# Kernel optimization log

Hardware: AMD Instinct MI355X
Metric: run time of the kernel (lower is better)

## Reference

```python
import jax, jax.numpy as jnp
import numpy as np

D_MODEL = 1024
NHEAD = 16
D_HEAD = D_MODEL // NHEAD


def setup_inputs() -> dict:
    key = jax.random.key(0)
    ks = jax.random.split(key, 11)
    B, S = 4, 1024
    s = 1.0 / np.sqrt(D_MODEL)
    inp = {
        'q_in': jax.random.normal(ks[0], (B, S, D_MODEL), jnp.float32),
        'k_in': jax.random.normal(ks[1], (B, S, D_MODEL), jnp.float32),
        'v_in': jax.random.normal(ks[2], (B, S, D_MODEL), jnp.float32),
        'Wq': jax.random.normal(ks[3], (D_MODEL, D_MODEL), jnp.float32) * s,
        'bq': jnp.zeros((D_MODEL,), jnp.float32),
        'Wk': jax.random.normal(ks[4], (D_MODEL, D_MODEL), jnp.float32) * s,
        'bk': jnp.zeros((D_MODEL,), jnp.float32),
        'Wv': jax.random.normal(ks[5], (D_MODEL, D_MODEL), jnp.float32) * s,
        'bv': jnp.zeros((D_MODEL,), jnp.float32),
        'Wo': jax.random.normal(ks[6], (D_MODEL, D_MODEL), jnp.float32) * s,
        'bo': jnp.zeros((D_MODEL,), jnp.float32),
    }
    return inp


def reference(q_in, k_in, v_in, Wq, bq, Wk, bk, Wv, bv, Wo, bo):
    B, Sq, _ = q_in.shape
    Sk = k_in.shape[1]
    # Linear projections (torch Linear: x @ W.T + b; here W stored as [in, out])
    Q = q_in @ Wq + bq
    K = k_in @ Wk + bk
    V = v_in @ Wv + bv
    # [B, H, S, Dh]
    Qh = Q.reshape(B, Sq, NHEAD, D_HEAD).transpose(0, 2, 1, 3)
    Kh = K.reshape(B, Sk, NHEAD, D_HEAD).transpose(0, 2, 1, 3)
    Vh = V.reshape(B, Sk, NHEAD, D_HEAD).transpose(0, 2, 1, 3)
    scores = jnp.einsum('bhqd,bhkd->bhqk', Qh, Kh) / jnp.sqrt(jnp.float32(D_HEAD))
    attn_weights = jax.nn.softmax(scores, axis=-1)
    attn = jnp.einsum('bhqk,bhkd->bhqd', attn_weights, Vh)
    attn = attn.transpose(0, 2, 1, 3).reshape(B, Sq, D_MODEL)
    out = attn @ Wo + bo
    return out
```

## Files before the change

kernel.cpp:

```cpp
#include <hip/hip_runtime.h>
#include <hip/hip_bf16.h>
#include <cstdint>
#include <cstddef>

typedef __bf16 bf16_t;
typedef __bf16 bf16x8 __attribute__((ext_vector_type(8)));
typedef __bf16 bf16x4 __attribute__((ext_vector_type(4)));
typedef float f32x4 __attribute__((ext_vector_type(4)));

#define DM 1024
#define NHEAD 16
#define DHEAD 64

#define QSCALE 0.18033688011112042f
#define PSHIFT 4.0f
#define RS 72

__device__ __forceinline__ void gload_lds16(const void* g, void* l) {
    __builtin_amdgcn_global_load_lds(
        (const __attribute__((address_space(1))) void*)g,
        (__attribute__((address_space(3))) void*)l,
        16, 0, 0);
}

__device__ __forceinline__ uint4 cvt8(float4 lo, float4 hi) {
    union { bf16_t b[8]; uint4 u; } o;
    o.b[0] = (bf16_t)lo.x; o.b[1] = (bf16_t)lo.y; o.b[2] = (bf16_t)lo.z; o.b[3] = (bf16_t)lo.w;
    o.b[4] = (bf16_t)hi.x; o.b[5] = (bf16_t)hi.y; o.b[6] = (bf16_t)hi.z; o.b[7] = (bf16_t)hi.w;
    return o.u;
}

__global__ void prep(
    const float* __restrict__ q_in, const float* __restrict__ k_in, const float* __restrict__ v_in,
    bf16_t* __restrict__ Xq, bf16_t* __restrict__ Xk, bf16_t* __restrict__ Xv,
    const float* __restrict__ w0, const float* __restrict__ w1,
    const float* __restrict__ w2, const float* __restrict__ w3,
    bf16_t* __restrict__ t0, bf16_t* __restrict__ t1,
    bf16_t* __restrict__ t2, bf16_t* __restrict__ t3)
{
    __shared__ float tile[32][33];
    int id = blockIdx.x;
    if (id < 6144) {
        int plane = id >> 11;
        int blk = id & 2047;
        const float* x = plane == 0 ? q_in : plane == 1 ? k_in : v_in;
        bf16_t* y      = plane == 0 ? Xq   : plane == 1 ? Xk   : Xv;
        int i = (blk * 256 + threadIdx.x) * 8;
        float4 lo = *(const float4*)&x[i];
        float4 hi = *(const float4*)&x[i + 4];
        *(uint4*)&y[i] = cvt8(lo, hi);
    } else {
        int t = id - 6144;
        int zi = t >> 10;
        int blk = t & 1023;
        const float* w = zi == 0 ? w0 : zi == 1 ? w1 : zi == 2 ? w2 : w3;
        bf16_t* wt     = zi == 0 ? t0 : zi == 1 ? t1 : zi == 2 ? t2 : t3;
        int bx = (blk & 31) * 32;
        int by = (blk >> 5) * 32;
        int tx = threadIdx.x & 31, ty = threadIdx.x >> 5;
        for (int j = 0; j < 32; j += 8)
            tile[ty + j][tx] = w[(size_t)(by + ty + j) * DM + bx + tx];
        __syncthreads();
        for (int j = 0; j < 32; j += 8)
            wt[(size_t)(bx + ty + j) * DM + by + tx] = (bf16_t)tile[tx][ty + j];
    }
}

template <int MODE>
__device__ __forceinline__ void gemm_body(
    const bf16_t* __restrict__ A, const bf16_t* __restrict__ Bt,
    const float* __restrict__ bias, float scale,
    float* __restrict__ Cf, bf16_t* __restrict__ Cb,
    int r0, int c0, bf16_t* AsP, bf16_t* BsP)
{
    const int K = 1024;
    int tid  = threadIdx.x;
    int wave = tid >> 6;
    int lane = tid & 63;
    int quad = lane >> 4;
    int ln   = lane & 15;
    int wr   = wave >> 1;
    int wc   = wave & 1;

    f32x4 acc[4][4];
    for (int rb = 0; rb < 4; rb++)
        for (int cb = 0; cb < 4; cb++)
            acc[rb][cb] = (f32x4){0.f, 0.f, 0.f, 0.f};

    int sr = tid >> 2;
    int sk = (tid & 3) * 8;

    const bf16_t* gA0 = &A[(size_t)(r0 + sr) * K + sk];
    const bf16_t* gA1 = gA0 + (size_t)64 * K;
    const bf16_t* gB0 = &Bt[(size_t)(c0 + sr) * K + sk];
    const bf16_t* gB1 = gB0 + (size_t)64 * K;
    char* lA = (char*)AsP + wave * 1024;
    char* lB = (char*)BsP + wave * 1024;

    gload_lds16(gA0, lA);
    gload_lds16(gA1, lA + 4096);
    gload_lds16(gB0, lB);
    gload_lds16(gB1, lB + 4096);
    __syncthreads();

    int cur = 0;
    for (int k0 = 0; k0 < K; k0 += 32) {
        int nxt = cur ^ 1;
        if (k0 + 32 < K) {
            int off = nxt * 8192;
            gload_lds16(gA0 + k0 + 32, lA + off);
            gload_lds16(gA1 + k0 + 32, lA + off + 4096);
            gload_lds16(gB0 + k0 + 32, lB + off);
            gload_lds16(gB1 + k0 + 32, lB + off + 4096);
        }
        const bf16_t* Ab = AsP + cur * 4096;
        const bf16_t* Bb = BsP + cur * 4096;

        bf16x8 af[4], bfv[4];
        for (int rb = 0; rb < 4; rb++)
            af[rb] = *(const bf16x8*)&Ab[(wr * 64 + rb * 16 + ln) * 32 + quad * 8];
        for (int cb = 0; cb < 4; cb++)
            bfv[cb] = *(const bf16x8*)&Bb[(wc * 64 + cb * 16 + ln) * 32 + quad * 8];
        for (int rb = 0; rb < 4; rb++)
            for (int cb = 0; cb < 4; cb++)
                acc[rb][cb] = __builtin_amdgcn_mfma_f32_16x16x32_bf16(af[rb], bfv[cb], acc[rb][cb], 0, 0, 0);

        __syncthreads();
        cur = nxt;
    }

    for (int rb = 0; rb < 4; rb++) {
        for (int cb = 0; cb < 4; cb++) {
            int C = c0 + wc * 64 + cb * 16 + ln;
            for (int r = 0; r < 4; r++) {
                int R = r0 + wr * 64 + rb * 16 + quad * 4 + r;
                float v = acc[rb][cb][r];
                if (MODE == 0) {
                    Cf[(size_t)R * DM + C] = v + bias[C];
                } else if (MODE == 1) {
                    int b = R >> 10, s = R & 1023;
                    int h = C >> 6,  d = C & 63;
                    Cb[(((size_t)b * NHEAD + h) * 1024 + s) * DHEAD + d] =
                        (bf16_t)((v + bias[C]) * scale);
                } else {
                    Cb[((size_t)(C >> 10) * 1024 + R) * 1024 + (C & 1023)] =
                        (bf16_t)(v + bias[R]);
                }
            }
        }
    }
}

__global__ __launch_bounds__(256) void gemm_qkv(
    const bf16_t* __restrict__ Xq, const bf16_t* __restrict__ Xk, const bf16_t* __restrict__ Xv,
    const bf16_t* __restrict__ Wtq, const bf16_t* __restrict__ Wtk, const bf16_t* __restrict__ Wtv,
    const float* __restrict__ bq, const float* __restrict__ bk, const float* __restrict__ bv,
    bf16_t* __restrict__ Qd, bf16_t* __restrict__ Kd, bf16_t* __restrict__ Vt)
{
    __shared__ __align__(16) bf16_t As[2 * 128 * 32];
    __shared__ __align__(16) bf16_t Bs[2 * 128 * 32];
    int z = blockIdx.z;
    if (z == 0) {
        gemm_body<1>(Xq, Wtq, bq, QSCALE, nullptr, Qd,
                     blockIdx.x * 128, blockIdx.y * 128, As, Bs);
    } else if (z == 1) {
        gemm_body<1>(Xk, Wtk, bk, 1.0f, nullptr, Kd,
                     blockIdx.x * 128, blockIdx.y * 128, As, Bs);
    } else {
        gemm_body<2>(Wtv, Xv, bv, 1.0f, nullptr, Vt,
                     blockIdx.y * 128, blockIdx.x * 128, As, Bs);
    }
}

__global__ __launch_bounds__(256) void gemm_out(
    const bf16_t* __restrict__ At, const bf16_t* __restrict__ Wto,
    const float* __restrict__ bo, float* __restrict__ out)
{
    const int K = 1024;
    __shared__ __align__(16) bf16_t As[2 * 64 * 32];
    __shared__ __align__(16) bf16_t Bs[2 * 128 * 32];

    int tid  = threadIdx.x;
    int wave = tid >> 6;
    int lane = tid & 63;
    int quad = lane >> 4;
    int ln   = lane & 15;

    int r0 = blockIdx.x * 64;
    int c0 = blockIdx.y * 128;

    f32x4 acc[4][2];
    for (int rb = 0; rb < 4; rb++)
        for (int cb = 0; cb < 2; cb++)
            acc[rb][cb] = (f32x4){0.f, 0.f, 0.f, 0.f};

    int sr = tid >> 2;
    int sk = (tid & 3) * 8;

    const bf16_t* gA0 = At  + (size_t)(r0 + sr) * K + sk;
    const bf16_t* gB0 = Wto + (size_t)(c0 + sr) * K + sk;
    const bf16_t* gB1 = gB0 + (size_t)64 * K;
    char* lA = (char*)As + wave * 1024;
    char* lB = (char*)Bs + wave * 1024;

    gload_lds16(gA0, lA);
    gload_lds16(gB0, lB);
    gload_lds16(gB1, lB + 4096);
    __syncthreads();

    int cur = 0;
    for (int k0 = 0; k0 < K; k0 += 32) {
        int nxt = cur ^ 1;
        if (k0 + 32 < K) {
            gload_lds16(gA0 + k0 + 32, lA + nxt * 4096);
            gload_lds16(gB0 + k0 + 32, lB + nxt * 8192);
            gload_lds16(gB1 + k0 + 32, lB + nxt * 8192 + 4096);
        }
        const bf16_t* Ab = As + cur * 2048;
        const bf16_t* Bb = Bs + cur * 4096;

        bf16x8 af[4], bfv[2];
        for (int rb = 0; rb < 4; rb++)
            af[rb] = *(const bf16x8*)&Ab[(rb * 16 + ln) * 32 + quad * 8];
        for (int cb = 0; cb < 2; cb++)
            bfv[cb] = *(const bf16x8*)&Bb[(wave * 32 + cb * 16 + ln) * 32 + quad * 8];
        for (int rb = 0; rb < 4; rb++)
            for (int cb = 0; cb < 2; cb++)
                acc[rb][cb] = __builtin_amdgcn_mfma_f32_16x16x32_bf16(af[rb], bfv[cb], acc[rb][cb], 0, 0, 0);

        __syncthreads();
        cur = nxt;
    }

    for (int rb = 0; rb < 4; rb++) {
        for (int cb = 0; cb < 2; cb++) {
            int C = c0 + wave * 32 + cb * 16 + ln;
            float bn = bo[C];
            for (int r = 0; r < 4; r++) {
                int R = r0 + rb * 16 + quad * 4 + r;
                out[(size_t)R * DM + C] = acc[rb][cb][r] + bn;
            }
        }
    }
}

__global__ __launch_bounds__(256) void attn5(
    const bf16_t* __restrict__ Q,
    const bf16_t* __restrict__ K,
    const bf16_t* __restrict__ Vt,
    bf16_t* __restrict__ O)
{
    __shared__ __align__(16) bf16_t Ks[64 * RS];
    __shared__ __align__(16) bf16_t Vs[64 * RS];
    __shared__ __align__(16) bf16_t Ps[4][16 * RS];

    int tid  = threadIdx.x;
    int wave = tid >> 6;
    int lane = tid & 63;
    int quad = lane >> 4;
    int ln   = lane & 15;

    int bh = blockIdx.x;
    int q0w = blockIdx.y * 64 + wave * 16;

    const bf16_t* Qb = Q  + (size_t)bh * 65536;
    const bf16_t* Kb = K  + (size_t)bh * 65536;
    const bf16_t* Vb = Vt + (size_t)bh * 65536;

    int srow = tid >> 3;
    int scol = (tid & 7) * 8;
    const bf16_t* gK0 = Kb + (size_t)srow * 64 + scol;
    const bf16_t* gK1 = gK0 + 32 * 64;
    const bf16_t* gV0 = Vb + (size_t)srow * 1024 + scol;
    const bf16_t* gV1 = gV0 + 32 * 1024;

    bf16x8 aq0 = *(const bf16x8*)&Qb[(size_t)(q0w + ln) * 64 + quad * 8];
    bf16x8 aq1 = *(const bf16x8*)&Qb[(size_t)(q0w + ln) * 64 + 32 + quad * 8];

    uint4 rK0 = *(const uint4*)gK0;
    uint4 rK1 = *(const uint4*)gK1;
    uint4 rV0 = *(const uint4*)gV0;
    uint4 rV1 = *(const uint4*)gV1;

    float l_lane = 0.f;
    f32x4 o_acc[4];
    for (int cb = 0; cb < 4; cb++) o_acc[cb] = (f32x4){0.f, 0.f, 0.f, 0.f};

    bf16_t* Pw = Ps[wave];

    for (int kt = 0; kt < 16; kt++) {
        __syncthreads();
        *(uint4*)&Ks[srow * RS + scol]        = rK0;
        *(uint4*)&Ks[(32 + srow) * RS + scol] = rK1;
        *(uint4*)&Vs[srow * RS + scol]        = rV0;
        *(uint4*)&Vs[(32 + srow) * RS + scol] = rV1;
        __syncthreads();

        if (kt < 15) {
            gK0 += 4096; gK1 += 4096; gV0 += 64; gV1 += 64;
            rK0 = *(const uint4*)gK0;
            rK1 = *(const uint4*)gK1;
            rV0 = *(const uint4*)gV0;
            rV1 = *(const uint4*)gV1;
        }

        f32x4 sc[4];
        for (int kb = 0; kb < 4; kb++) {
            bf16x8 kf0 = *(const bf16x8*)&Ks[(kb * 16 + ln) * RS + quad * 8];
            bf16x8 kf1 = *(const bf16x8*)&Ks[(kb * 16 + ln) * RS + 32 + quad * 8];
            f32x4 a = (f32x4){0.f, 0.f, 0.f, 0.f};
            a = __builtin_amdgcn_mfma_f32_16x16x32_bf16(kf0, aq0, a, 0, 0, 0);
            a = __builtin_amdgcn_mfma_f32_16x16x32_bf16(kf1, aq1, a, 0, 0, 0);
            sc[kb] = a;
        }

        for (int kb = 0; kb < 4; kb++) {
            float p0 = __builtin_amdgcn_exp2f(sc[kb][0] - PSHIFT);
            float p1 = __builtin_amdgcn_exp2f(sc[kb][1] - PSHIFT);
            float p2 = __builtin_amdgcn_exp2f(sc[kb][2] - PSHIFT);
            float p3 = __builtin_amdgcn_exp2f(sc[kb][3] - PSHIFT);
            l_lane += (p0 + p1) + (p2 + p3);
            bf16x4 pk = (bf16x4){(bf16_t)p0, (bf16_t)p1, (bf16_t)p2, (bf16_t)p3};
            *(bf16x4*)&Pw[ln * RS + kb * 16 + quad * 4] = pk;
        }

        for (int kc = 0; kc < 2; kc++) {
            bf16x8 ap = *(const bf16x8*)&Pw[ln * RS + kc * 32 + quad * 8];
            for (int cb = 0; cb < 4; cb++) {
                bf16x8 vf = *(const bf16x8*)&Vs[(cb * 16 + ln) * RS + kc * 32 + quad * 8];
                o_acc[cb] = __builtin_amdgcn_mfma_f32_16x16x32_bf16(ap, vf, o_acc[cb], 0, 0, 0);
            }
        }
    }

    float l = l_lane;
    l += __shfl_xor(l, 16);
    l += __shfl_xor(l, 32);
    float invq[4];
    for (int r = 0; r < 4; r++)
        invq[r] = 1.f / __shfl(l, quad * 4 + r);

    int b = bh >> 4, h = bh & 15;
    for (int cb = 0; cb < 4; cb++) {
        for (int r = 0; r < 4; r++) {
            int q = q0w + quad * 4 + r;
            int d = cb * 16 + ln;
            O[((size_t)b * 1024 + q) * DM + h * 64 + d] = (bf16_t)(o_acc[cb][r] * invq[r]);
        }
    }
}

extern "C" void kernel_launch(void* const* d_in, const int* in_sizes, int n_in,
                              void* d_out, int out_size, void* d_ws, size_t ws_size,
                              hipStream_t stream) {
    const float* q_in = (const float*)d_in[0];
    const float* k_in = (const float*)d_in[1];
    const float* v_in = (const float*)d_in[2];
    const float* Wq   = (const float*)d_in[3];
    const float* bq   = (const float*)d_in[4];
    const float* Wk   = (const float*)d_in[5];
    const float* bk   = (const float*)d_in[6];
    const float* Wv   = (const float*)d_in[7];
    const float* bv   = (const float*)d_in[8];
    const float* Wo   = (const float*)d_in[9];
    const float* bo   = (const float*)d_in[10];

    char* ws = (char*)d_ws;
    const size_t MB = 1024ull * 1024ull;
    bf16_t* Xq  = (bf16_t*)(ws);
    bf16_t* Xk  = (bf16_t*)(ws + 8 * MB);
    bf16_t* Xv  = (bf16_t*)(ws + 16 * MB);
    bf16_t* Wtq = (bf16_t*)(ws + 24 * MB);
    bf16_t* Wtk = (bf16_t*)(ws + 26 * MB);
    bf16_t* Wtv = (bf16_t*)(ws + 28 * MB);
    bf16_t* Wto = (bf16_t*)(ws + 30 * MB);
    bf16_t* Qd  = (bf16_t*)(ws + 32 * MB);
    bf16_t* Kd  = (bf16_t*)(ws + 40 * MB);
    bf16_t* Vt  = (bf16_t*)(ws + 48 * MB);
    bf16_t* At  = Xq;

    prep<<<10240, 256, 0, stream>>>(q_in, k_in, v_in, Xq, Xk, Xv,
                                    Wq, Wk, Wv, Wo, Wtq, Wtk, Wtv, Wto);

    gemm_qkv<<<dim3(32, 8, 3), 256, 0, stream>>>(Xq, Xk, Xv,
                                                 Wtq, Wtk, Wtv, bq, bk, bv, Qd, Kd, Vt);

    attn5<<<dim3(64, 16), 256, 0, stream>>>(Qd, Kd, Vt, At);

    gemm_out<<<dim3(64, 8), 256, 0, stream>>>(At, Wto, bo, (float*)d_out);
}
```

Before: 208.4 us.

## Double query rows per attention wave and widen weight-transpose tiles

The attention kernel now has each wave process 32 query rows instead of 16, so every K/V tile staged in shared memory is reused by twice as many queries. This halves the grid and the K/V global traffic per query. Separately, the weight transpose in the prep kernel uses 64x64 tiles with 16-byte vectorized bf16 stores instead of 32x32 tiles with scalar stores. The cost is more registers per wave and fewer attention blocks in flight, which may lower occupancy and latency hiding.

```diff
diff --git a/kernel.cpp b/kernel.cpp
--- a/kernel.cpp
+++ b/kernel.cpp
@@ -38,7 +38,7 @@
     bf16_t* __restrict__ t0, bf16_t* __restrict__ t1,
     bf16_t* __restrict__ t2, bf16_t* __restrict__ t3)
 {
-    __shared__ float tile[32][33];
+    __shared__ float tile[64][65];
     int id = blockIdx.x;
     if (id < 6144) {
         int plane = id >> 11;
@@ -51,18 +51,25 @@
         *(uint4*)&y[i] = cvt8(lo, hi);
     } else {
         int t = id - 6144;
-        int zi = t >> 10;
-        int blk = t & 1023;
+        int zi = t >> 8;
+        int blk = t & 255;
         const float* w = zi == 0 ? w0 : zi == 1 ? w1 : zi == 2 ? w2 : w3;
         bf16_t* wt     = zi == 0 ? t0 : zi == 1 ? t1 : zi == 2 ? t2 : t3;
-        int bx = (blk & 31) * 32;
-        int by = (blk >> 5) * 32;
-        int tx = threadIdx.x & 31, ty = threadIdx.x >> 5;
-        for (int j = 0; j < 32; j += 8)
+        int bx = (blk & 15) * 64;
+        int by = (blk >> 4) * 64;
+        int tx = threadIdx.x & 63, ty = threadIdx.x >> 6;
+        for (int j = 0; j < 64; j += 4)
             tile[ty + j][tx] = w[(size_t)(by + ty + j) * DM + bx + tx];
         __syncthreads();
-        for (int j = 0; j < 32; j += 8)
-            wt[(size_t)(bx + ty + j) * DM + by + tx] = (bf16_t)tile[tx][ty + j];
+        int nl = threadIdx.x >> 3;
+        int kl = (threadIdx.x & 7) * 8;
+        for (int j = 0; j < 64; j += 32) {
+            int n = nl + j;
+            union { bf16_t b[8]; uint4 u; } o;
+            for (int i = 0; i < 8; i++)
+                o.b[i] = (bf16_t)tile[kl + i][n];
+            *(uint4*)&wt[(size_t)(bx + n) * DM + by + kl] = o.u;
+        }
     }
 }
 
@@ -244,7 +251,7 @@
     }
 }
 
-__global__ __launch_bounds__(256) void attn5(
+__global__ __launch_bounds__(256) void attn6(
     const bf16_t* __restrict__ Q,
     const bf16_t* __restrict__ K,
     const bf16_t* __restrict__ Vt,
@@ -252,7 +259,7 @@
 {
     __shared__ __align__(16) bf16_t Ks[64 * RS];
     __shared__ __align__(16) bf16_t Vs[64 * RS];
-    __shared__ __align__(16) bf16_t Ps[4][16 * RS];
+    __shared__ __align__(16) bf16_t Ps[4][32 * RS];
 
     int tid  = threadIdx.x;
     int wave = tid >> 6;
@@ -261,7 +268,7 @@
     int ln   = lane & 15;
 
     int bh = blockIdx.x;
-    int q0w = blockIdx.y * 64 + wave * 16;
+    int q0w = blockIdx.y * 128 + wave * 32;
 
     const bf16_t* Qb = Q  + (size_t)bh * 65536;
     const bf16_t* Kb = K  + (size_t)bh * 65536;
@@ -274,17 +281,22 @@
     const bf16_t* gV0 = Vb + (size_t)srow * 1024 + scol;
     const bf16_t* gV1 = gV0 + 32 * 1024;
 
-    bf16x8 aq0 = *(const bf16x8*)&Qb[(size_t)(q0w + ln) * 64 + quad * 8];
-    bf16x8 aq1 = *(const bf16x8*)&Qb[(size_t)(q0w + ln) * 64 + 32 + quad * 8];
+    bf16x8 aq0[2], aq1[2];
+    for (int h = 0; h < 2; h++) {
+        aq0[h] = *(const bf16x8*)&Qb[(size_t)(q0w + h * 16 + ln) * 64 + quad * 8];
+        aq1[h] = *(const bf16x8*)&Qb[(size_t)(q0w + h * 16 + ln) * 64 + 32 + quad * 8];
+    }
 
     uint4 rK0 = *(const uint4*)gK0;
     uint4 rK1 = *(const uint4*)gK1;
     uint4 rV0 = *(const uint4*)gV0;
     uint4 rV1 = *(const uint4*)gV1;
 
-    float l_lane = 0.f;
-    f32x4 o_acc[4];
-    for (int cb = 0; cb < 4; cb++) o_acc[cb] = (f32x4){0.f, 0.f, 0.f, 0.f};
+    float l_lane[2] = {0.f, 0.f};
+    f32x4 o_acc[2][4];
+    for (int h = 0; h < 2; h++)
+        for (int cb = 0; cb < 4; cb++)
+            o_acc[h][cb] = (f32x4){0.f, 0.f, 0.f, 0.f};
 
     bf16_t* Pw = Ps[wave];
 
@@ -304,48 +316,55 @@
             rV1 = *(const uint4*)gV1;
         }
 
-        f32x4 sc[4];
+        f32x4 sc[4][2];
         for (int kb = 0; kb < 4; kb++) {
             bf16x8 kf0 = *(const bf16x8*)&Ks[(kb * 16 + ln) * RS + quad * 8];
             bf16x8 kf1 = *(const bf16x8*)&Ks[(kb * 16 + ln) * RS + 32 + quad * 8];
-            f32x4 a = (f32x4){0.f, 0.f, 0.f, 0.f};
-            a = __builtin_amdgcn_mfma_f32_16x16x32_bf16(kf0, aq0, a, 0, 0, 0);
-            a = __builtin_amdgcn_mfma_f32_16x16x32_bf16(kf1, aq1, a, 0, 0, 0);
-            sc[kb] = a;
+            for (int h = 0; h < 2; h++) {
+                f32x4 a = (f32x4){0.f, 0.f, 0.f, 0.f};
+                a = __builtin_amdgcn_mfma_f32_16x16x32_bf16(kf0, aq0[h], a, 0, 0, 0);
+                a = __builtin_amdgcn_mfma_f32_16x16x32_bf16(kf1, aq1[h], a, 0, 0, 0);
+                sc[kb][h] = a;
+            }
         }
 
         for (int kb = 0; kb < 4; kb++) {
-            float p0 = __builtin_amdgcn_exp2f(sc[kb][0] - PSHIFT);
-            float p1 = __builtin_amdgcn_exp2f(sc[kb][1] - PSHIFT);
-            float p2 = __builtin_amdgcn_exp2f(sc[kb][2] - PSHIFT);
-            float p3 = __builtin_amdgcn_exp2f(sc[kb][3] - PSHIFT);
-            l_lane += (p0 + p1) + (p2 + p3);
-            bf16x4 pk = (bf16x4){(bf16_t)p0, (bf16_t)p1, (bf16_t)p2, (bf16_t)p3};
-            *(bf16x4*)&Pw[ln * RS + kb * 16 + quad * 4] = pk;
+            for (int h = 0; h < 2; h++) {
+                float p0 = __builtin_amdgcn_exp2f(sc[kb][h][0] - PSHIFT);
+                float p1 = __builtin_amdgcn_exp2f(sc[kb][h][1] - PSHIFT);
+                float p2 = __builtin_amdgcn_exp2f(sc[kb][h][2] - PSHIFT);
+                float p3 = __builtin_amdgcn_exp2f(sc[kb][h][3] - PSHIFT);
+                l_lane[h] += (p0 + p1) + (p2 + p3);
+                bf16x4 pk = (bf16x4){(bf16_t)p0, (bf16_t)p1, (bf16_t)p2, (bf16_t)p3};
+                *(bf16x4*)&Pw[(h * 16 + ln) * RS + kb * 16 + quad * 4] = pk;
+            }
         }
 
         for (int kc = 0; kc < 2; kc++) {
-            bf16x8 ap = *(const bf16x8*)&Pw[ln * RS + kc * 32 + quad * 8];
+            bf16x8 ap0 = *(const bf16x8*)&Pw[ln * RS + kc * 32 + quad * 8];
+            bf16x8 ap1 = *(const bf16x8*)&Pw[(16 + ln) * RS + kc * 32 + quad * 8];
             for (int cb = 0; cb < 4; cb++) {
                 bf16x8 vf = *(const bf16x8*)&Vs[(cb * 16 + ln) * RS + kc * 32 + quad * 8];
-                o_acc[cb] = __builtin_amdgcn_mfma_f32_16x16x32_bf16(ap, vf, o_acc[cb], 0, 0, 0);
-            }
-        }
-    }
-
-    float l = l_lane;
-    l += __shfl_xor(l, 16);
-    l += __shfl_xor(l, 32);
-    float invq[4];
-    for (int r = 0; r < 4; r++)
-        invq[r] = 1.f / __shfl(l, quad * 4 + r);
-
-    int b = bh >> 4, h = bh & 15;
-    for (int cb = 0; cb < 4; cb++) {
-        for (int r = 0; r < 4; r++) {
-            int q = q0w + quad * 4 + r;
-            int d = cb * 16 + ln;
-            O[((size_t)b * 1024 + q) * DM + h * 64 + d] = (bf16_t)(o_acc[cb][r] * invq[r]);
+                o_acc[0][cb] = __builtin_amdgcn_mfma_f32_16x16x32_bf16(ap0, vf, o_acc[0][cb], 0, 0, 0);
+                o_acc[1][cb] = __builtin_amdgcn_mfma_f32_16x16x32_bf16(ap1, vf, o_acc[1][cb], 0, 0, 0);
+            }
+        }
+    }
+
+    int b = bh >> 4, hd = bh & 15;
+    for (int h = 0; h < 2; h++) {
+        float l = l_lane[h];
+        l += __shfl_xor(l, 16);
+        l += __shfl_xor(l, 32);
+        float invq[4];
+        for (int r = 0; r < 4; r++)
+            invq[r] = 1.f / __shfl(l, quad * 4 + r);
+        for (int cb = 0; cb < 4; cb++) {
+            for (int r = 0; r < 4; r++) {
+                int q = q0w + h * 16 + quad * 4 + r;
+                int d = cb * 16 + ln;
+                O[((size_t)b * 1024 + q) * DM + hd * 64 + d] = (bf16_t)(o_acc[h][cb][r] * invq[r]);
+            }
         }
     }
 }
@@ -379,13 +398,13 @@
     bf16_t* Vt  = (bf16_t*)(ws + 48 * MB);
     bf16_t* At  = Xq;
 
-    prep<<<10240, 256, 0, stream>>>(q_in, k_in, v_in, Xq, Xk, Xv,
-                                    Wq, Wk, Wv, Wo, Wtq, Wtk, Wtv, Wto);
+    prep<<<7168, 256, 0, stream>>>(q_in, k_in, v_in, Xq, Xk, Xv,
+                                   Wq, Wk, Wv, Wo, Wtq, Wtk, Wtv, Wto);
 
     gemm_qkv<<<dim3(32, 8, 3), 256, 0, stream>>>(Xq, Xk, Xv,
                                                  Wtq, Wtk, Wtv, bq, bk, bv, Qd, Kd, Vt);
 
-    attn5<<<dim3(64, 16), 256, 0, stream>>>(Qd, Kd, Vt, At);
+    attn6<<<dim3(64, 8), 256, 0, stream>>>(Qd, Kd, Vt, At);
 
     gemm_out<<<dim3(64, 8), 256, 0, stream>>>(At, Wto, bo, (float*)d_out);
 }
```

Result: faster. 203.7 us (-2.3%).
